# Kernel optimization log

Measured on AMD Instinct MI355X. Metric: run time of the kernel, lower is better.

The kernel has to match this reference:

```python
import jax, jax.numpy as jnp
import numpy as np

ISIZE = 1024
OSIZE = 1024
EPS = 1e-5  # torch nn.LayerNorm default


def setup_inputs() -> dict:
    key = jax.random.key(0)
    k0, k1, k2 = jax.random.split(key, 3)
    B, S = 32, 256
    x = jax.random.normal(k0, (B, S, ISIZE), dtype=jnp.float32)
    # Linear(isize + osize, 4*osize): W stored as (in, out) for x @ W
    scale = 1.0 / np.sqrt(ISIZE + OSIZE)
    W = jax.random.uniform(k1, (ISIZE + OSIZE, 4 * OSIZE), dtype=jnp.float32,
                           minval=-scale, maxval=scale)
    b = jax.random.uniform(k2, (4 * OSIZE,), dtype=jnp.float32,
                           minval=-scale, maxval=scale)
    gamma = jnp.ones((4, OSIZE), dtype=jnp.float32)   # LayerNorm((4, osize)) weight
    beta = jnp.zeros((4, OSIZE), dtype=jnp.float32)   # LayerNorm((4, osize)) bias
    init_hx = jnp.zeros((1, OSIZE), dtype=jnp.float32)
    init_cx = jnp.zeros((1, OSIZE), dtype=jnp.float32)
    return {"x": x, "W": W, "b": b, "gamma": gamma, "beta": beta,
            "init_hx": init_hx, "init_cx": init_cx}


def _layernorm_2d(z, gamma, beta):
    # Normalize jointly over the last two dims (4, osize), per torch LayerNorm((4, osize))
    mean = jnp.mean(z, axis=(-2, -1), keepdims=True)
    var = jnp.var(z, axis=(-2, -1), keepdims=True)
    return (z - mean) * jax.lax.rsqrt(var + EPS) * gamma + beta


def reference(x, W, b, gamma, beta, init_hx, init_cx):
    B, S, _ = x.shape
    osize = init_hx.shape[-1]
    hx = jnp.broadcast_to(init_hx, (B, osize))  # prepare_initState: expand to batch
    cx = jnp.broadcast_to(init_cx, (B, osize))

    def step(carry, xt):
        h, c = carry
        comb = jnp.concatenate([xt, h], axis=-1) @ W + b       # [B, 4*osize]
        comb = _layernorm_2d(comb.reshape(B, 4, osize), gamma, beta)
        ig, fg, hidden, og = comb[:, 0], comb[:, 1], comb[:, 2], comb[:, 3]
        c = jax.nn.sigmoid(fg) * c + jax.nn.sigmoid(ig) * jnp.tanh(hidden)
        h = jax.nn.sigmoid(og) * c                              # RNMT+ cell: out = og * cell
        return (h, c), h

    xs = jnp.swapaxes(x, 0, 1)                                  # [S, B, isize]
    _, outs = jax.lax.scan(step, (hx, cx), xs)
    return jnp.swapaxes(outs, 0, 1)                             # [B, S, osize]
```

## Files before the change

### kernel.cpp

```cpp
#include <hip/hip_runtime.h>
#include <hip/hip_bf16.h>

#define NB 32
#define NS 256
#define NI 1024
#define NO 1024
#define NK 2048
#define NC 4096
#define LN_EPS 1e-5f

typedef __attribute__((ext_vector_type(4))) float f32x4;
typedef __attribute__((ext_vector_type(4))) unsigned int u32x4;

__device__ __forceinline__ f32x4 mfma_bf16_16x16x32(u32x4 a, u32x4 b, f32x4 c) {
  asm volatile("v_mfma_f32_16x16x32_bf16 %0, %1, %2, %0" : "+v"(c) : "v"(a), "v"(b));
  return c;
}

__device__ __forceinline__ float sigf(float x) { return 1.0f / (1.0f + __expf(-x)); }
__device__ __forceinline__ float tanhfast(float x) {
  return 1.0f - 2.0f / (__expf(2.0f * x) + 1.0f);
}


__global__ void pack_x(const float* __restrict__ x, __hip_bfloat16* __restrict__ xfrag) {
  const int t = blockIdx.x, kt = blockIdx.y;
  const int tid = threadIdx.x;
  const int plane = tid >> 6, l = tid & 63, q = (l >> 4), ln = l & 15;
  const int m = plane * 16 + ln;
  const float* src = x + ((size_t)m * NS + t) * NI + kt * 32 + q * 8;
  float4 v0 = *(const float4*)src;
  float4 v1 = *(const float4*)(src + 4);
  __align__(16) __hip_bfloat16 tmp[8];
  tmp[0] = __float2bfloat16(v0.x); tmp[1] = __float2bfloat16(v0.y);
  tmp[2] = __float2bfloat16(v0.z); tmp[3] = __float2bfloat16(v0.w);
  tmp[4] = __float2bfloat16(v1.x); tmp[5] = __float2bfloat16(v1.y);
  tmp[6] = __float2bfloat16(v1.z); tmp[7] = __float2bfloat16(v1.w);
  *(u32x4*)(xfrag + (((size_t)t * 32 + kt) * 2 + plane) * 512 + l * 8) = *(const u32x4*)tmp;
}

__global__ void pack_wf(const float* __restrict__ W, __hip_bfloat16* __restrict__ WF) {
  const int blk = blockIdx.x;
  const int b = blk >> 6, kt = blk & 63;
  const int l = threadIdx.x, q = l >> 4, c = l & 15;
  const int n  = ((c >> 2) << 10) + b * 4 + (c & 3);
  const int k0 = kt * 32 + q * 8;
  __align__(16) __hip_bfloat16 tmp[8];
#pragma unroll
  for (int j = 0; j < 8; ++j)
    tmp[j] = __float2bfloat16(W[(size_t)(k0 + j) * NC + n]);
  *(u32x4*)(WF + ((size_t)(b * 64 + kt) * 64 + l) * 8) = *(const u32x4*)tmp;
}

__device__ __forceinline__ size_t hfrag_idx(int m, int j) {
  const int kt = j >> 5, q = (j >> 3) & 3, jj = j & 7;
  const int plane = m >> 4, l = q * 16 + (m & 15);
  return (((size_t)kt * 2 + plane) * 64 + l) * 8 + jj;
}

__global__ void init_state(const float* __restrict__ hx0, const float* __restrict__ cx0,
                           __hip_bfloat16* __restrict__ hfrag, float* __restrict__ cst,
                           float* __restrict__ hf) {
  const int i = blockIdx.x * 256 + threadIdx.x;
  const int m = i >> 10, j = i & (NO - 1);
  const float hv = hx0[j];
  hfrag[hfrag_idx(m, j)] = __float2bfloat16(hv);
  hf[i]  = hv;
  cst[i] = cx0[j];
}

__global__ __launch_bounds__(512)
void step_gemm_mfma(const __hip_bfloat16* __restrict__ xfrag,
                    const __hip_bfloat16* __restrict__ hfrag,
                    const __hip_bfloat16* __restrict__ WF,
                    const float* __restrict__ bias,
                    float* __restrict__ comb, int t) {
  __shared__ __align__(16) float xch[8 * 2 * 256];
  const int b = blockIdx.x, tid = threadIdx.x;
  const int wv = tid >> 6, l = tid & 63;

  const __hip_bfloat16* ap = (wv < 4)
      ? xfrag + ((size_t)t * 32 + wv * 8) * 1024 + l * 8
      : hfrag + ((size_t)(wv - 4) * 8) * 1024 + l * 8;
  const __hip_bfloat16* bp = WF + ((size_t)(b * 64 + wv * 8) * 64 + l) * 8;

  f32x4 acc0 = {0.f, 0.f, 0.f, 0.f}, acc1 = {0.f, 0.f, 0.f, 0.f};
  asm volatile("s_nop 1" ::);
#pragma unroll
  for (int i = 0; i < 8; ++i) {
    u32x4 a0 = *(const u32x4*)(ap + (size_t)i * 1024);
    u32x4 a1 = *(const u32x4*)(ap + (size_t)i * 1024 + 512);
    u32x4 bb = *(const u32x4*)(bp + (size_t)i * 512);
    acc0 = mfma_bf16_16x16x32(a0, bb, acc0);
    acc1 = mfma_bf16_16x16x32(a1, bb, acc1);
  }
  asm volatile("s_nop 7\n\ts_nop 7" ::);

  *(f32x4*)(xch + (wv * 2 + 0) * 256 + l * 4) = acc0;
  *(f32x4*)(xch + (wv * 2 + 1) * 256 + l * 4) = acc1;
  __syncthreads();

  const int row = tid >> 4, c = tid & 15;
  const int p = row >> 4, rr = row & 15;
  const int idx = ((rr >> 2) * 16 + c) * 4 + (rr & 3);
  const int n = ((c >> 2) << 10) + b * 4 + (c & 3);
  float v = bias[n];
#pragma unroll
  for (int w = 0; w < 8; ++w) v += xch[(w * 2 + p) * 256 + idx];
  comb[(size_t)row * NC + n] = v;
}

__global__ __launch_bounds__(1024)
void step_update_row(const float* __restrict__ comb,
                     const float* __restrict__ gamma,
                     const float* __restrict__ beta,
                     float* __restrict__ cst,
                     float* __restrict__ out,
                     __hip_bfloat16* __restrict__ hfrag,
                     int t) {
  __shared__ __align__(16) float combL[NC];
  __shared__ float red[16][2];
  __shared__ float stat[2];
  const int m = blockIdx.x, tid = threadIdx.x;

  f32x4 cv = *(const f32x4*)(comb + (size_t)m * NC + tid * 4);
  *(f32x4*)(combL + tid * 4) = cv;
  float s  = cv[0] + cv[1] + cv[2] + cv[3];
  float ss = cv[0] * cv[0] + cv[1] * cv[1] + cv[2] * cv[2] + cv[3] * cv[3];
#pragma unroll
  for (int off = 1; off < 64; off <<= 1) {
    s  += __shfl_xor(s, off);
    ss += __shfl_xor(ss, off);
  }
  const int wid = tid >> 6;
  if ((tid & 63) == 0) { red[wid][0] = s; red[wid][1] = ss; }
  __syncthreads();
  if (tid == 0) {
    float s2 = 0.f, ss2 = 0.f;
#pragma unroll
    for (int i = 0; i < 16; ++i) { s2 += red[i][0]; ss2 += red[i][1]; }
    const float mean = s2 * (1.f / NC);
    const float var  = ss2 * (1.f / NC) - mean * mean;
    stat[0] = mean;
    stat[1] = rsqrtf(var + LN_EPS);
  }
  __syncthreads();
  const float mean = stat[0], rs = stat[1];
  const int j = tid;
  const float iv = (combL[j]          - mean) * rs * gamma[j]          + beta[j];
  const float fv = (combL[NO + j]     - mean) * rs * gamma[NO + j]     + beta[NO + j];
  const float gv = (combL[2 * NO + j] - mean) * rs * gamma[2 * NO + j] + beta[2 * NO + j];
  const float ov = (combL[3 * NO + j] - mean) * rs * gamma[3 * NO + j] + beta[3 * NO + j];
  const float cold = cst[(size_t)m * NO + j];
  const float cc = sigf(fv) * cold + sigf(iv) * tanhfast(gv);
  const float hh = sigf(ov) * cc;
  cst[(size_t)m * NO + j] = cc;
  out[((size_t)m * NS + t) * NO + j] = hh;
  hfrag[hfrag_idx(m, j)] = __float2bfloat16(hh);
}


__launch_bounds__(256)
__global__ void step_gemm_f32(const float* __restrict__ x, const float* __restrict__ hf,
                              const float* __restrict__ W, const float* __restrict__ bias,
                              float* __restrict__ comb, int t) {
  const int blk = blockIdx.x;
  const int tid = threadIdx.x;
  const int n   = blk * 16 + (tid & 15);
  const int mlo = tid >> 4;
  float a0 = 0.f, a1 = 0.f;
  for (int k = 0; k < NI; ++k) {
    const float wv = W[(size_t)k * NC + n];
    a0 += x[((size_t)mlo * NS + t) * NI + k] * wv;
    a1 += x[((size_t)(mlo + 16) * NS + t) * NI + k] * wv;
  }
  for (int k = 0; k < NO; ++k) {
    const float wv = W[(size_t)(NI + k) * NC + n];
    a0 += hf[mlo * NO + k] * wv;
    a1 += hf[(mlo + 16) * NO + k] * wv;
  }
  comb[(size_t)mlo * NC + n] = a0 + bias[n];
  comb[(size_t)(mlo + 16) * NC + n] = a1 + bias[n];
}

__global__ __launch_bounds__(1024)
void step_update_row_f32(const float* __restrict__ comb,
                         const float* __restrict__ gamma,
                         const float* __restrict__ beta,
                         float* __restrict__ cst,
                         float* __restrict__ out,
                         float* __restrict__ hf,
                         int t) {
  __shared__ __align__(16) float combL[NC];
  __shared__ float red[16][2];
  __shared__ float stat[2];
  const int m = blockIdx.x, tid = threadIdx.x;
  f32x4 cv = *(const f32x4*)(comb + (size_t)m * NC + tid * 4);
  *(f32x4*)(combL + tid * 4) = cv;
  float s  = cv[0] + cv[1] + cv[2] + cv[3];
  float ss = cv[0] * cv[0] + cv[1] * cv[1] + cv[2] * cv[2] + cv[3] * cv[3];
#pragma unroll
  for (int off = 1; off < 64; off <<= 1) {
    s  += __shfl_xor(s, off);
    ss += __shfl_xor(ss, off);
  }
  const int wid = tid >> 6;
  if ((tid & 63) == 0) { red[wid][0] = s; red[wid][1] = ss; }
  __syncthreads();
  if (tid == 0) {
    float s2 = 0.f, ss2 = 0.f;
    for (int i = 0; i < 16; ++i) { s2 += red[i][0]; ss2 += red[i][1]; }
    const float mean = s2 * (1.f / NC);
    const float var  = ss2 * (1.f / NC) - mean * mean;
    stat[0] = mean;
    stat[1] = rsqrtf(var + LN_EPS);
  }
  __syncthreads();
  const float mean = stat[0], rs = stat[1];
  const int j = tid;
  const float iv = (combL[j]          - mean) * rs * gamma[j]          + beta[j];
  const float fv = (combL[NO + j]     - mean) * rs * gamma[NO + j]     + beta[NO + j];
  const float gv = (combL[2 * NO + j] - mean) * rs * gamma[2 * NO + j] + beta[2 * NO + j];
  const float ov = (combL[3 * NO + j] - mean) * rs * gamma[3 * NO + j] + beta[3 * NO + j];
  const float cold = cst[(size_t)m * NO + j];
  const float cc = sigf(fv) * cold + sigf(iv) * tanhfast(gv);
  const float hh = sigf(ov) * cc;
  cst[(size_t)m * NO + j] = cc;
  out[((size_t)m * NS + t) * NO + j] = hh;
  hf[(size_t)m * NO + j] = hh;
}


extern "C" void kernel_launch(void* const* d_in, const int* in_sizes, int n_in,
                              void* d_out, int out_size, void* d_ws, size_t ws_size,
                              hipStream_t stream) {
  (void)in_sizes; (void)n_in; (void)out_size;
  const float* x     = (const float*)d_in[0];
  const float* W     = (const float*)d_in[1];
  const float* bias  = (const float*)d_in[2];
  const float* gamma = (const float*)d_in[3];
  const float* beta  = (const float*)d_in[4];
  const float* hx0   = (const float*)d_in[5];
  const float* cx0   = (const float*)d_in[6];
  float* outp = (float*)d_out;

  char* ws = (char*)d_ws;
  size_t off = 0;
  auto alloc = [&](size_t bytes) -> char* {
    off = (off + 255) & ~(size_t)255;
    char* p = ws + off;
    off += bytes;
    return p;
  };
  float* comb          = (float*)alloc((size_t)NB * NC * 4);
  float* cst           = (float*)alloc((size_t)NB * NO * 4);
  float* hf            = (float*)alloc((size_t)NB * NO * 4);
  __hip_bfloat16* hfrag = (__hip_bfloat16*)alloc((size_t)NB * NO * 2);
  __hip_bfloat16* xfrag = (__hip_bfloat16*)alloc((size_t)NB * NS * NI * 2);
  __hip_bfloat16* WF    = (__hip_bfloat16*)alloc((size_t)NK * NC * 2);
  const bool big = (ws_size >= off);

  hipLaunchKernelGGL(init_state, dim3((NB * NO) / 256), dim3(256), 0, stream,
                     hx0, cx0, hfrag, cst, hf);
  if (big) {
    hipLaunchKernelGGL(pack_x, dim3(NS, 32), dim3(128), 0, stream, x, xfrag);
    hipLaunchKernelGGL(pack_wf, dim3(256 * 64), dim3(64), 0, stream, W, WF);
    for (int t = 0; t < NS; ++t) {
      hipLaunchKernelGGL(step_gemm_mfma, dim3(256), dim3(512), 0, stream,
                         xfrag, hfrag, WF, bias, comb, t);
      hipLaunchKernelGGL(step_update_row, dim3(NB), dim3(1024), 0, stream,
                         comb, gamma, beta, cst, outp, hfrag, t);
    }
  } else {
    for (int t = 0; t < NS; ++t) {
      hipLaunchKernelGGL(step_gemm_f32, dim3(256), dim3(256), 0, stream,
                         x, hf, W, bias, comb, t);
      hipLaunchKernelGGL(step_update_row_f32, dim3(NB), dim3(1024), 0, stream,
                         comb, gamma, beta, cst, outp, hf, t);
    }
  }
}
```

Measured before the change: 2.448 ms.

## Fuse recurrent LSTM steps into one persistent cooperative kernel with global flags

Replaces the per-timestep pair of kernel launches (GEMM then layernorm/update) with a single cooperative persistent kernel that loops over all timesteps. Each block keeps its weight fragments in registers for the whole run and sums layernorm statistics through global atomics. Blocks synchronise on the hidden state through coherent loads and spin-polled counters. This removes 512 launches and repeated weight loads, at the cost of spin-wait latency, atomic traffic and a dependence on all 256 blocks being co-resident. One wave per block is reserved for the cell update, and the x-projection is split unevenly across the other three waves.

```diff
diff --git a/kernel.cpp b/kernel.cpp
--- a/kernel.cpp
+++ b/kernel.cpp
@@ -8,6 +8,7 @@
 #define NK 2048
 #define NC 4096
 #define LN_EPS 1e-5f
+#define SPIN_GUARD (1 << 18)
 
 typedef __attribute__((ext_vector_type(4))) float f32x4;
 typedef __attribute__((ext_vector_type(4))) unsigned int u32x4;
@@ -20,6 +21,49 @@
 __device__ __forceinline__ float sigf(float x) { return 1.0f / (1.0f + __expf(-x)); }
 __device__ __forceinline__ float tanhfast(float x) {
   return 1.0f - 2.0f / (__expf(2.0f * x) + 1.0f);
+}
+
+__device__ __forceinline__ unsigned int load_coh_u32(const void* p) {
+  unsigned int v;
+  asm volatile("global_load_dword %0, %1, off sc0 sc1\n\ts_waitcnt vmcnt(0)"
+               : "=&v"(v) : "v"(p));
+  return v;
+}
+__device__ __forceinline__ float load_coh_f32(const void* p) {
+  float v;
+  asm volatile("global_load_dword %0, %1, off sc0 sc1\n\ts_waitcnt vmcnt(0)"
+               : "=&v"(v) : "v"(p));
+  return v;
+}
+__device__ __forceinline__ void atomic_swap_coh_u32(void* p, unsigned int v) {
+  asm volatile("global_atomic_swap %0, %1, off sc1" :: "v"(p), "v"(v) : "memory");
+}
+__device__ __forceinline__ void atomic_add_coh_u32(void* p, unsigned int v) {
+  asm volatile("global_atomic_add %0, %1, off sc1" :: "v"(p), "v"(v) : "memory");
+}
+__device__ __forceinline__ void atomic_add_coh_f32(void* p, float v) {
+  asm volatile("global_atomic_add_f32 %0, %1, off sc1" :: "v"(p), "v"(v) : "memory");
+}
+#define COH_LOAD8(d, a0,a1,a2,a3,a4,a5,a6,a7)                          \
+  asm volatile(                                                         \
+    "global_load_dwordx4 %0, %8, off sc0 sc1\n\t"                      \
+    "global_load_dwordx4 %1, %9, off sc0 sc1\n\t"                      \
+    "global_load_dwordx4 %2, %10, off sc0 sc1\n\t"                     \
+    "global_load_dwordx4 %3, %11, off sc0 sc1\n\t"                     \
+    "global_load_dwordx4 %4, %12, off sc0 sc1\n\t"                     \
+    "global_load_dwordx4 %5, %13, off sc0 sc1\n\t"                     \
+    "global_load_dwordx4 %6, %14, off sc0 sc1\n\t"                     \
+    "global_load_dwordx4 %7, %15, off sc0 sc1\n\t"                     \
+    "s_waitcnt vmcnt(0)"                                                \
+    : "=&v"(d[0]), "=&v"(d[1]), "=&v"(d[2]), "=&v"(d[3]),               \
+      "=&v"(d[4]), "=&v"(d[5]), "=&v"(d[6]), "=&v"(d[7])                \
+    : "v"(a0), "v"(a1), "v"(a2), "v"(a3), "v"(a4), "v"(a5), "v"(a6), "v"(a7))
+
+__device__ __forceinline__ void poll_coh_ge(const unsigned int* p, unsigned int target) {
+  for (int g = 0; g < SPIN_GUARD; ++g) {
+    if (load_coh_u32(p) >= target) return;
+    __builtin_amdgcn_s_sleep(2);
+  }
 }
 
 
@@ -59,104 +103,183 @@
 }
 
 __global__ void init_state(const float* __restrict__ hx0, const float* __restrict__ cx0,
-                           __hip_bfloat16* __restrict__ hfrag, float* __restrict__ cst,
-                           float* __restrict__ hf) {
+                           float* __restrict__ cst, float* __restrict__ hf) {
   const int i = blockIdx.x * 256 + threadIdx.x;
-  const int m = i >> 10, j = i & (NO - 1);
-  const float hv = hx0[j];
-  hfrag[hfrag_idx(m, j)] = __float2bfloat16(hv);
-  hf[i]  = hv;
+  const int j = i & (NO - 1);
+  hf[i]  = hx0[j];
   cst[i] = cx0[j];
 }
 
 __global__ __launch_bounds__(512)
-void step_gemm_mfma(const __hip_bfloat16* __restrict__ xfrag,
-                    const __hip_bfloat16* __restrict__ hfrag,
-                    const __hip_bfloat16* __restrict__ WF,
-                    const float* __restrict__ bias,
-                    float* __restrict__ comb, int t) {
+void lstm_persistent(const __hip_bfloat16* __restrict__ xfrag,
+                     __hip_bfloat16* __restrict__ hfrag,
+                     const __hip_bfloat16* __restrict__ WF,
+                     const float* __restrict__ bias,
+                     const float* __restrict__ gamma,
+                     const float* __restrict__ beta,
+                     const float* __restrict__ hx0,
+                     const float* __restrict__ cx0,
+                     float* __restrict__ out,
+                     float* __restrict__ srow,
+                     unsigned int* __restrict__ scnt,
+                     unsigned int* __restrict__ hcnt) {
   __shared__ __align__(16) float xch[8 * 2 * 256];
+  __shared__ __align__(16) float combB[32 * 16];
+  __shared__ int hgo;
+
   const int b = blockIdx.x, tid = threadIdx.x;
   const int wv = tid >> 6, l = tid & 63;
 
-  const __hip_bfloat16* ap = (wv < 4)
-      ? xfrag + ((size_t)t * 32 + wv * 8) * 1024 + l * 8
-      : hfrag + ((size_t)(wv - 4) * 8) * 1024 + l * 8;
-  const __hip_bfloat16* bp = WF + ((size_t)(b * 64 + wv * 8) * 64 + l) * 8;
-
-  f32x4 acc0 = {0.f, 0.f, 0.f, 0.f}, acc1 = {0.f, 0.f, 0.f, 0.f};
-  asm volatile("s_nop 1" ::);
-#pragma unroll
-  for (int i = 0; i < 8; ++i) {
-    u32x4 a0 = *(const u32x4*)(ap + (size_t)i * 1024);
-    u32x4 a1 = *(const u32x4*)(ap + (size_t)i * 1024 + 512);
-    u32x4 bb = *(const u32x4*)(bp + (size_t)i * 512);
-    acc0 = mfma_bf16_16x16x32(a0, bb, acc0);
-    acc1 = mfma_bf16_16x16x32(a1, bb, acc1);
-  }
-  asm volatile("s_nop 7\n\ts_nop 7" ::);
-
-  *(f32x4*)(xch + (wv * 2 + 0) * 256 + l * 4) = acc0;
-  *(f32x4*)(xch + (wv * 2 + 1) * 256 + l * 4) = acc1;
-  __syncthreads();
+  int kt0, nkt;
+  if (wv == 0)      { kt0 = 0; nkt = 0; }
+  else if (wv < 4)  { kt0 = (wv - 1) * 11; nkt = (wv == 3) ? 10 : 11; }
+  else              { kt0 = 32 + (wv - 4) * 8; nkt = 8; }
+
+  u32x4 bb[11];
+  {
+    const __hip_bfloat16* bp = WF + ((size_t)(b * 64 + kt0) * 64 + l) * 8;
+#pragma unroll
+    for (int i = 0; i < 11; ++i)
+      if (i < nkt) bb[i] = *(const u32x4*)(bp + (size_t)i * 512);
+  }
 
   const int row = tid >> 4, c = tid & 15;
   const int p = row >> 4, rr = row & 15;
   const int idx = ((rr >> 2) * 16 + c) * 4 + (rr & 3);
   const int n = ((c >> 2) << 10) + b * 4 + (c & 3);
-  float v = bias[n];
-#pragma unroll
-  for (int w = 0; w < 8; ++w) v += xch[(w * 2 + p) * 256 + idx];
-  comb[(size_t)row * NC + n] = v;
-}
-
-__global__ __launch_bounds__(1024)
-void step_update_row(const float* __restrict__ comb,
-                     const float* __restrict__ gamma,
-                     const float* __restrict__ beta,
-                     float* __restrict__ cst,
-                     float* __restrict__ out,
-                     __hip_bfloat16* __restrict__ hfrag,
-                     int t) {
-  __shared__ __align__(16) float combL[NC];
-  __shared__ float red[16][2];
-  __shared__ float stat[2];
-  const int m = blockIdx.x, tid = threadIdx.x;
-
-  f32x4 cv = *(const f32x4*)(comb + (size_t)m * NC + tid * 4);
-  *(f32x4*)(combL + tid * 4) = cv;
-  float s  = cv[0] + cv[1] + cv[2] + cv[3];
-  float ss = cv[0] * cv[0] + cv[1] * cv[1] + cv[2] * cv[2] + cv[3] * cv[3];
-#pragma unroll
-  for (int off = 1; off < 64; off <<= 1) {
-    s  += __shfl_xor(s, off);
-    ss += __shfl_xor(ss, off);
-  }
-  const int wid = tid >> 6;
-  if ((tid & 63) == 0) { red[wid][0] = s; red[wid][1] = ss; }
+  const float bn = bias[n];
+
+  const int gm = l >> 1, gh = l & 1;
+  const int j0 = b * 4 + 2 * gh;
+  float ga[4][2], be[4][2];
+  float c0 = 0.f, c1 = 0.f;
+  if (wv == 0) {
+#pragma unroll
+    for (int g = 0; g < 4; ++g) {
+      ga[g][0] = gamma[g * NO + j0]; ga[g][1] = gamma[g * NO + j0 + 1];
+      be[g][0] = beta[g * NO + j0];  be[g][1] = beta[g * NO + j0 + 1];
+    }
+    c0 = cx0[j0]; c1 = cx0[j0 + 1];
+  }
+  if (tid == 0) hgo = 0;
   __syncthreads();
-  if (tid == 0) {
-    float s2 = 0.f, ss2 = 0.f;
-#pragma unroll
-    for (int i = 0; i < 16; ++i) { s2 += red[i][0]; ss2 += red[i][1]; }
-    const float mean = s2 * (1.f / NC);
-    const float var  = ss2 * (1.f / NC) - mean * mean;
-    stat[0] = mean;
-    stat[1] = rsqrtf(var + LN_EPS);
-  }
-  __syncthreads();
-  const float mean = stat[0], rs = stat[1];
-  const int j = tid;
-  const float iv = (combL[j]          - mean) * rs * gamma[j]          + beta[j];
-  const float fv = (combL[NO + j]     - mean) * rs * gamma[NO + j]     + beta[NO + j];
-  const float gv = (combL[2 * NO + j] - mean) * rs * gamma[2 * NO + j] + beta[2 * NO + j];
-  const float ov = (combL[3 * NO + j] - mean) * rs * gamma[3 * NO + j] + beta[3 * NO + j];
-  const float cold = cst[(size_t)m * NO + j];
-  const float cc = sigf(fv) * cold + sigf(iv) * tanhfast(gv);
-  const float hh = sigf(ov) * cc;
-  cst[(size_t)m * NO + j] = cc;
-  out[((size_t)m * NS + t) * NO + j] = hh;
-  hfrag[hfrag_idx(m, j)] = __float2bfloat16(hh);
+
+  for (int t = 0; t < NS; ++t) {
+    f32x4 acc0 = {0.f, 0.f, 0.f, 0.f}, acc1 = {0.f, 0.f, 0.f, 0.f};
+    asm volatile("s_nop 1" ::);
+    if (wv >= 1 && wv < 4) {
+      const __hip_bfloat16* ap = xfrag + ((size_t)t * 32 + kt0) * 1024 + l * 8;
+#pragma unroll
+      for (int i = 0; i < 11; ++i)
+        if (i < nkt) {
+          u32x4 a0 = *(const u32x4*)(ap + (size_t)i * 1024);
+          u32x4 a1 = *(const u32x4*)(ap + (size_t)i * 1024 + 512);
+          acc0 = mfma_bf16_16x16x32(a0, bb[i], acc0);
+          acc1 = mfma_bf16_16x16x32(a1, bb[i], acc1);
+        }
+    } else if (wv >= 4) {
+      u32x4 ha[8], hb[8];
+      if (t == 0) {
+        const int q = l >> 4;
+#pragma unroll
+        for (int i = 0; i < 8; ++i) {
+          const int k0 = ((wv - 4) * 8 + i) * 32 + q * 8;
+          float4 v0 = *(const float4*)(hx0 + k0);
+          float4 v1 = *(const float4*)(hx0 + k0 + 4);
+          __align__(16) __hip_bfloat16 tmp[8];
+          tmp[0] = __float2bfloat16(v0.x); tmp[1] = __float2bfloat16(v0.y);
+          tmp[2] = __float2bfloat16(v0.z); tmp[3] = __float2bfloat16(v0.w);
+          tmp[4] = __float2bfloat16(v1.x); tmp[5] = __float2bfloat16(v1.y);
+          tmp[6] = __float2bfloat16(v1.z); tmp[7] = __float2bfloat16(v1.w);
+          ha[i] = *(const u32x4*)tmp;
+          hb[i] = ha[i];
+        }
+      } else {
+        if (wv == 4) {
+          poll_coh_ge(hcnt + t, 256u);
+          if (l == 0)
+            __hip_atomic_store(&hgo, t, __ATOMIC_RELEASE, __HIP_MEMORY_SCOPE_WORKGROUP);
+        } else {
+          for (int g = 0; g < SPIN_GUARD; ++g) {
+            if (__hip_atomic_load(&hgo, __ATOMIC_ACQUIRE, __HIP_MEMORY_SCOPE_WORKGROUP) >= t)
+              break;
+            __builtin_amdgcn_s_sleep(1);
+          }
+        }
+        __builtin_amdgcn_sched_barrier(0);
+        const __hip_bfloat16* ap = hfrag + ((size_t)(wv - 4) * 8) * 1024 + l * 8;
+        COH_LOAD8(ha, ap + (size_t)0 * 1024, ap + (size_t)1 * 1024,
+                      ap + (size_t)2 * 1024, ap + (size_t)3 * 1024,
+                      ap + (size_t)4 * 1024, ap + (size_t)5 * 1024,
+                      ap + (size_t)6 * 1024, ap + (size_t)7 * 1024);
+        COH_LOAD8(hb, ap + (size_t)0 * 1024 + 512, ap + (size_t)1 * 1024 + 512,
+                      ap + (size_t)2 * 1024 + 512, ap + (size_t)3 * 1024 + 512,
+                      ap + (size_t)4 * 1024 + 512, ap + (size_t)5 * 1024 + 512,
+                      ap + (size_t)6 * 1024 + 512, ap + (size_t)7 * 1024 + 512);
+        __builtin_amdgcn_sched_barrier(0);
+      }
+#pragma unroll
+      for (int i = 0; i < 8; ++i) {
+        acc0 = mfma_bf16_16x16x32(ha[i], bb[i], acc0);
+        acc1 = mfma_bf16_16x16x32(hb[i], bb[i], acc1);
+      }
+    }
+    asm volatile("s_nop 7\n\ts_nop 7" ::);
+
+    if (wv >= 1) {
+      *(f32x4*)(xch + (wv * 2 + 0) * 256 + l * 4) = acc0;
+      *(f32x4*)(xch + (wv * 2 + 1) * 256 + l * 4) = acc1;
+    }
+    __syncthreads();
+
+    float v = bn;
+#pragma unroll
+    for (int w = 1; w < 8; ++w) v += xch[(w * 2 + p) * 256 + idx];
+    combB[row * 16 + c] = v;
+    float s = v, ss = v * v;
+#pragma unroll
+    for (int off = 1; off < 16; off <<= 1) {
+      s  += __shfl_xor(s, off);
+      ss += __shfl_xor(ss, off);
+    }
+    if (c == 0) {
+      atomic_add_coh_f32(srow + ((size_t)t * 32 + row) * 2 + 0, s);
+      atomic_add_coh_f32(srow + ((size_t)t * 32 + row) * 2 + 1, ss);
+    }
+    asm volatile("s_waitcnt vmcnt(0)" ::: "memory");
+    __syncthreads();
+    if (tid == 0) atomic_add_coh_u32(scnt + t, 1u);
+
+    if (wv == 0) {
+      poll_coh_ge(scnt + t, 256u);
+      __builtin_amdgcn_sched_barrier(0);
+      const float sv  = load_coh_f32(srow + ((size_t)t * 32 + gm) * 2 + 0);
+      const float ssv = load_coh_f32(srow + ((size_t)t * 32 + gm) * 2 + 1);
+      const float mean = sv * (1.f / NC);
+      const float var  = ssv * (1.f / NC) - mean * mean;
+      const float rs = rsqrtf(var + LN_EPS);
+      const int cb = 2 * gh;
+      float pre[4][2];
+#pragma unroll
+      for (int g = 0; g < 4; ++g) {
+        pre[g][0] = (combB[gm * 16 + g * 4 + cb]     - mean) * rs * ga[g][0] + be[g][0];
+        pre[g][1] = (combB[gm * 16 + g * 4 + cb + 1] - mean) * rs * ga[g][1] + be[g][1];
+      }
+      const float cc0 = sigf(pre[1][0]) * c0 + sigf(pre[0][0]) * tanhfast(pre[2][0]);
+      const float cc1 = sigf(pre[1][1]) * c1 + sigf(pre[0][1]) * tanhfast(pre[2][1]);
+      const float hh0 = sigf(pre[3][0]) * cc0;
+      const float hh1 = sigf(pre[3][1]) * cc1;
+      c0 = cc0; c1 = cc1;
+      float2 o2; o2.x = hh0; o2.y = hh1;
+      *(float2*)(out + ((size_t)gm * NS + t) * NO + j0) = o2;
+      __hip_bfloat16 hb0 = __float2bfloat16(hh0), hb1 = __float2bfloat16(hh1);
+      unsigned int hp = (unsigned int)*(unsigned short*)&hb0 |
+                        ((unsigned int)*(unsigned short*)&hb1 << 16);
+      atomic_swap_coh_u32((void*)(hfrag + hfrag_idx(gm, j0)), hp);
+      asm volatile("s_waitcnt vmcnt(0)" ::: "memory");
+      if (l == 0) atomic_add_coh_u32(hcnt + t + 1, 1u);
+    }
+  }
 }
 
 
@@ -256,22 +379,27 @@
   float* cst           = (float*)alloc((size_t)NB * NO * 4);
   float* hf            = (float*)alloc((size_t)NB * NO * 4);
   __hip_bfloat16* hfrag = (__hip_bfloat16*)alloc((size_t)NB * NO * 2);
+  float* srow          = (float*)alloc((size_t)NS * 32 * 2 * 4);
+  unsigned int* scnt   = (unsigned int*)alloc((size_t)NS * 4);
+  unsigned int* hcnt   = (unsigned int*)alloc((size_t)(NS + 1) * 4);
   __hip_bfloat16* xfrag = (__hip_bfloat16*)alloc((size_t)NB * NS * NI * 2);
   __hip_bfloat16* WF    = (__hip_bfloat16*)alloc((size_t)NK * NC * 2);
   const bool big = (ws_size >= off);
 
-  hipLaunchKernelGGL(init_state, dim3((NB * NO) / 256), dim3(256), 0, stream,
-                     hx0, cx0, hfrag, cst, hf);
   if (big) {
+    hipMemsetAsync(srow, 0, (size_t)NS * 32 * 2 * 4, stream);
+    hipMemsetAsync(scnt, 0, (size_t)NS * 4, stream);
+    hipMemsetAsync(hcnt, 0, (size_t)(NS + 1) * 4, stream);
     hipLaunchKernelGGL(pack_x, dim3(NS, 32), dim3(128), 0, stream, x, xfrag);
     hipLaunchKernelGGL(pack_wf, dim3(256 * 64), dim3(64), 0, stream, W, WF);
-    for (int t = 0; t < NS; ++t) {
-      hipLaunchKernelGGL(step_gemm_mfma, dim3(256), dim3(512), 0, stream,
-                         xfrag, hfrag, WF, bias, comb, t);
-      hipLaunchKernelGGL(step_update_row, dim3(NB), dim3(1024), 0, stream,
-                         comb, gamma, beta, cst, outp, hfrag, t);
-    }
+    void* args[] = {(void*)&xfrag, (void*)&hfrag, (void*)&WF, (void*)&bias,
+                    (void*)&gamma, (void*)&beta, (void*)&hx0, (void*)&cx0,
+                    (void*)&outp, (void*)&srow, (void*)&scnt, (void*)&hcnt};
+    hipLaunchCooperativeKernel((void*)lstm_persistent, dim3(256), dim3(512),
+                               args, 0, stream);
   } else {
+    hipLaunchKernelGGL(init_state, dim3((NB * NO) / 256), dim3(256), 0, stream,
+                       hx0, cx0, cst, hf);
     for (int t = 0; t < NS; ++t) {
       hipLaunchKernelGGL(step_gemm_f32, dim3(256), dim3(256), 0, stream,
                          x, hf, W, bias, comb, t);
```

Result: slower. 9.516 ms (+288.8%).

## Precompute input projection for all timesteps before the recurrent loop

Applied to the files above, without the earlier changes.

Adds a kernel that computes x_t·W_x plus bias for every timestep in one launch and stores the result as bf16 in a large workspace buffer. Each recurrent step then only multiplies h by the recurrent half of W and adds the precomputed term, halving the K dimension on the serial critical path. The path is used only when the workspace holds the extra 64MB buffer; otherwise it falls back to the previous fused per-step GEMM. Rounding the x-projection to bf16 adds some precision loss.

```diff
diff --git a/kernel.cpp b/kernel.cpp
--- a/kernel.cpp
+++ b/kernel.cpp
@@ -67,6 +67,88 @@
   hfrag[hfrag_idx(m, j)] = __float2bfloat16(hv);
   hf[i]  = hv;
   cst[i] = cx0[j];
+}
+
+__global__ __launch_bounds__(512)
+void xgemm_all(const __hip_bfloat16* __restrict__ xfrag,
+               const __hip_bfloat16* __restrict__ WF,
+               const float* __restrict__ bias,
+               __hip_bfloat16* __restrict__ xa) {
+  __shared__ __align__(16) float xch[8 * 2 * 256];
+  const int b = blockIdx.x, tid = threadIdx.x;
+  const int wv = tid >> 6, l = tid & 63;
+  const int kt0 = wv * 4;
+  u32x4 bb[4];
+  {
+    const __hip_bfloat16* bp = WF + ((size_t)(b * 64 + kt0) * 64 + l) * 8;
+#pragma unroll
+    for (int i = 0; i < 4; ++i) bb[i] = *(const u32x4*)(bp + (size_t)i * 512);
+  }
+  const int row = tid >> 4, c = tid & 15;
+  const int p = row >> 4, rr = row & 15;
+  const int idx = ((rr >> 2) * 16 + c) * 4 + (rr & 3);
+  const int n = ((c >> 2) << 10) + b * 4 + (c & 3);
+  const float bn = bias[n];
+
+  for (int t = 0; t < NS; ++t) {
+    f32x4 acc0 = {0.f, 0.f, 0.f, 0.f}, acc1 = {0.f, 0.f, 0.f, 0.f};
+    asm volatile("s_nop 1" ::);
+    const __hip_bfloat16* ap = xfrag + ((size_t)t * 32 + kt0) * 1024 + l * 8;
+#pragma unroll
+    for (int i = 0; i < 4; ++i) {
+      u32x4 a0 = *(const u32x4*)(ap + (size_t)i * 1024);
+      u32x4 a1 = *(const u32x4*)(ap + (size_t)i * 1024 + 512);
+      acc0 = mfma_bf16_16x16x32(a0, bb[i], acc0);
+      acc1 = mfma_bf16_16x16x32(a1, bb[i], acc1);
+    }
+    asm volatile("s_nop 7\n\ts_nop 7" ::);
+    *(f32x4*)(xch + (wv * 2 + 0) * 256 + l * 4) = acc0;
+    *(f32x4*)(xch + (wv * 2 + 1) * 256 + l * 4) = acc1;
+    __syncthreads();
+    float v = bn;
+#pragma unroll
+    for (int w = 0; w < 8; ++w) v += xch[(w * 2 + p) * 256 + idx];
+    xa[((size_t)t * 256 + b) * 512 + tid] = __float2bfloat16(v);
+    __syncthreads();
+  }
+}
+
+__global__ __launch_bounds__(512)
+void step_gemm_h(const __hip_bfloat16* __restrict__ hfrag,
+                 const __hip_bfloat16* __restrict__ WF,
+                 const __hip_bfloat16* __restrict__ xa,
+                 float* __restrict__ comb, int t) {
+  __shared__ __align__(16) float xch[8 * 2 * 256];
+  const int b = blockIdx.x, tid = threadIdx.x;
+  const int wv = tid >> 6, l = tid & 63;
+  const int kt0 = wv * 4;
+  const __hip_bfloat16* ap = hfrag + (size_t)kt0 * 1024 + l * 8;
+  const __hip_bfloat16* bp = WF + ((size_t)(b * 64 + 32 + kt0) * 64 + l) * 8;
+
+  f32x4 acc0 = {0.f, 0.f, 0.f, 0.f}, acc1 = {0.f, 0.f, 0.f, 0.f};
+  asm volatile("s_nop 1" ::);
+#pragma unroll
+  for (int i = 0; i < 4; ++i) {
+    u32x4 a0 = *(const u32x4*)(ap + (size_t)i * 1024);
+    u32x4 a1 = *(const u32x4*)(ap + (size_t)i * 1024 + 512);
+    u32x4 bbv = *(const u32x4*)(bp + (size_t)i * 512);
+    acc0 = mfma_bf16_16x16x32(a0, bbv, acc0);
+    acc1 = mfma_bf16_16x16x32(a1, bbv, acc1);
+  }
+  asm volatile("s_nop 7\n\ts_nop 7" ::);
+
+  *(f32x4*)(xch + (wv * 2 + 0) * 256 + l * 4) = acc0;
+  *(f32x4*)(xch + (wv * 2 + 1) * 256 + l * 4) = acc1;
+  __syncthreads();
+
+  const int row = tid >> 4, c = tid & 15;
+  const int p = row >> 4, rr = row & 15;
+  const int idx = ((rr >> 2) * 16 + c) * 4 + (rr & 3);
+  const int n = ((c >> 2) << 10) + b * 4 + (c & 3);
+  float v = __bfloat162float(xa[((size_t)t * 256 + b) * 512 + tid]);
+#pragma unroll
+  for (int w = 0; w < 8; ++w) v += xch[(w * 2 + p) * 256 + idx];
+  comb[(size_t)row * NC + n] = v;
 }
 
 __global__ __launch_bounds__(512)
@@ -252,17 +334,35 @@
     off += bytes;
     return p;
   };
-  float* comb          = (float*)alloc((size_t)NB * NC * 4);
-  float* cst           = (float*)alloc((size_t)NB * NO * 4);
-  float* hf            = (float*)alloc((size_t)NB * NO * 4);
+  float* comb           = (float*)alloc((size_t)NB * NC * 4);
+  float* cst            = (float*)alloc((size_t)NB * NO * 4);
+  float* hf             = (float*)alloc((size_t)NB * NO * 4);
   __hip_bfloat16* hfrag = (__hip_bfloat16*)alloc((size_t)NB * NO * 2);
   __hip_bfloat16* xfrag = (__hip_bfloat16*)alloc((size_t)NB * NS * NI * 2);
   __hip_bfloat16* WF    = (__hip_bfloat16*)alloc((size_t)NK * NC * 2);
-  const bool big = (ws_size >= off);
-
-  hipLaunchKernelGGL(init_state, dim3((NB * NO) / 256), dim3(256), 0, stream,
-                     hx0, cx0, hfrag, cst, hf);
-  if (big) {
+  const size_t off_tier2 = off;
+  __hip_bfloat16* xa    = (__hip_bfloat16*)alloc((size_t)NS * NB * NC * 2);
+  const size_t off_tier1 = off;
+
+  const bool tier1 = (ws_size >= off_tier1);
+  const bool tier2 = (ws_size >= off_tier2);
+
+  if (tier1) {
+    hipLaunchKernelGGL(init_state, dim3((NB * NO) / 256), dim3(256), 0, stream,
+                       hx0, cx0, hfrag, cst, hf);
+    hipLaunchKernelGGL(pack_x, dim3(NS, 32), dim3(128), 0, stream, x, xfrag);
+    hipLaunchKernelGGL(pack_wf, dim3(256 * 64), dim3(64), 0, stream, W, WF);
+    hipLaunchKernelGGL(xgemm_all, dim3(256), dim3(512), 0, stream,
+                       xfrag, WF, bias, xa);
+    for (int t = 0; t < NS; ++t) {
+      hipLaunchKernelGGL(step_gemm_h, dim3(256), dim3(512), 0, stream,
+                         hfrag, WF, xa, comb, t);
+      hipLaunchKernelGGL(step_update_row, dim3(NB), dim3(1024), 0, stream,
+                         comb, gamma, beta, cst, outp, hfrag, t);
+    }
+  } else if (tier2) {
+    hipLaunchKernelGGL(init_state, dim3((NB * NO) / 256), dim3(256), 0, stream,
+                       hx0, cx0, hfrag, cst, hf);
     hipLaunchKernelGGL(pack_x, dim3(NS, 32), dim3(128), 0, stream, x, xfrag);
     hipLaunchKernelGGL(pack_wf, dim3(256 * 64), dim3(64), 0, stream, W, WF);
     for (int t = 0; t < NS; ++t) {
@@ -272,6 +372,8 @@
                          comb, gamma, beta, cst, outp, hfrag, t);
     }
   } else {
+    hipLaunchKernelGGL(init_state, dim3((NB * NO) / 256), dim3(256), 0, stream,
+                       hx0, cx0, hfrag, cst, hf);
     for (int t = 0; t < NS; ++t) {
       hipLaunchKernelGGL(step_gemm_f32, dim3(256), dim3(256), 0, stream,
                          x, hf, W, bias, comb, t);
```

After: 2.497 ms. 2.0% more time.
